# Kernel tuning notes

Measured on AMD Instinct MI355X. Metric: run time of the kernel, lower is better.

## Reference

```python
import jax, jax.numpy as jnp
import numpy as np

B, S, DIM = 2, 2048, 2048
H = 16
Q_LORA, KV_LORA = 768, 512
NOPE, ROPE, VD = 128, 64, 128
QKD = NOPE + ROPE  # 192
SOFTCAP = 30.0
EPS = 1e-6
NEG = -1e9
SCALE = QKD ** -0.5  # max_seq_len <= original_seq_len -> no mscale correction


def rms_norm(x, w, eps=EPS):
    xf = x.astype(jnp.float32)
    y = xf * jax.lax.rsqrt(jnp.mean(xf * xf, axis=-1, keepdims=True) + eps)
    return (y * w.astype(jnp.float32)).astype(x.dtype)


def apply_rope(x, cos, sin):
    # x: [B, S, H, D] with interleaved (even, odd) pairs; cos/sin: [S, D//2]
    xr = x.astype(jnp.float32).reshape(*x.shape[:-1], -1, 2)
    xe, xo = xr[..., 0], xr[..., 1]
    c = cos[None, :, None, :]
    s = sin[None, :, None, :]
    ye = xe * c - xo * s
    yo = xe * s + xo * c
    return jnp.stack([ye, yo], axis=-1).reshape(x.shape).astype(x.dtype)


def setup_inputs():
    key = jax.random.key(0)
    ks = jax.random.split(key, 6)
    def w(k, shape, fan_in):
        return jax.random.normal(k, shape, jnp.float32) * (fan_in ** -0.5)
    x = jax.random.normal(ks[0], (B, S, DIM), jnp.float32)
    wq_a_w = w(ks[1], (Q_LORA, DIM), DIM)
    wq_b_w = w(ks[2], (H * QKD, Q_LORA), Q_LORA)
    wkv_a_w = w(ks[3], (KV_LORA + ROPE, DIM), DIM)
    wkv_b_w = w(ks[4], (H * (NOPE + VD), KV_LORA), KV_LORA)
    wo_w = w(ks[5], (DIM, H * VD), H * VD)
    q_norm_w = jnp.ones((Q_LORA,), jnp.float32)
    kv_norm_w = jnp.ones((KV_LORA,), jnp.float32)
    q_gain = jnp.full((H,), 1.5, jnp.float32)  # qk_gain_init
    inv_freq = 1.0 / (10000.0 ** (np.arange(0, ROPE, 2, dtype=np.float32) / ROPE))
    fr = np.outer(np.arange(S, dtype=np.float32), inv_freq)  # [S, 32]
    freqs_cos = jnp.asarray(np.cos(fr))
    freqs_sin = jnp.asarray(np.sin(fr))
    mask = jnp.asarray(np.where(np.triu(np.ones((S, S), dtype=bool), 1), NEG, 0.0).astype(np.float32))
    return dict(x=x, wq_a_w=wq_a_w, q_norm_w=q_norm_w, wq_b_w=wq_b_w, q_gain=q_gain,
                wkv_a_w=wkv_a_w, kv_norm_w=kv_norm_w, wkv_b_w=wkv_b_w, wo_w=wo_w,
                freqs_cos=freqs_cos, freqs_sin=freqs_sin, mask=mask, start_pos=0)


def reference(x, wq_a_w, q_norm_w, wq_b_w, q_gain, wkv_a_w, kv_norm_w, wkv_b_w, wo_w,
              freqs_cos, freqs_sin, mask, start_pos):
    b, s, _ = x.shape
    # low-rank Q: wq_a -> RMSNorm -> wq_b
    q = rms_norm(x @ wq_a_w.T, q_norm_w) @ wq_b_w.T          # [B,S,H*QKD]
    q = q.reshape(b, s, H, QKD)
    q_nope, q_pe = q[..., :NOPE], q[..., NOPE:]
    q_pe = apply_rope(q_pe, freqs_cos, freqs_sin)            # rope_dims=0 -> full 64-dim rotation
    q_pe = q_pe * q_gain[None, None, :, None]                # learned per-head QK gain
    # low-rank KV + decoupled rope key
    kv_full = x @ wkv_a_w.T                                  # [B,S,KV_LORA+ROPE]
    kv, k_pe = kv_full[..., :KV_LORA], kv_full[..., KV_LORA:]
    kv = rms_norm(kv, kv_norm_w)
    k_pe = apply_rope(k_pe[:, :, None, :], freqs_cos, freqs_sin)  # [B,S,1,ROPE]
    # prefill (mask is not None) branch: expand latent kv through wkv_b
    kvb = (kv @ wkv_b_w.T).reshape(b, s, H, NOPE + VD)
    k_nope, v = kvb[..., :NOPE], kvb[..., NOPE:]
    k = jnp.concatenate([k_nope, jnp.broadcast_to(k_pe, (b, s, H, ROPE))], axis=-1)
    qf = jnp.concatenate([q_nope, q_pe], axis=-1)            # [B,S,H,QKD]
    scores = jnp.einsum('bshd,bthd->bsht', qf, k) * SCALE
    scores = SOFTCAP * jnp.tanh(scores / SOFTCAP)            # logit softcap
    scores = scores + mask[None, :, None, :]                 # causal additive mask [S,T]
    p = jax.nn.softmax(scores.astype(jnp.float32), axis=-1).astype(x.dtype)
    y = jnp.einsum('bsht,bthd->bshd', p, v)                  # [B,S,H,VD]
    # XSA: subtract self-value projection
    vn = v * jax.lax.rsqrt(jnp.maximum(jnp.sum(v * v, axis=-1, keepdims=True), 1e-12))
    y = y - jnp.sum(y * vn, axis=-1, keepdims=True) * vn
    return y.reshape(b, s, H * VD) @ wo_w.T                  # [B,S,DIM]
```

## Files before the change

### kernel.cpp

```cpp
#include <hip/hip_runtime.h>
#include <stdint.h>

typedef unsigned short u16;
typedef __bf16 bf16x8 __attribute__((ext_vector_type(8)));
typedef float f32x4 __attribute__((ext_vector_type(4)));
typedef unsigned int u32x4 __attribute__((ext_vector_type(4)));
typedef unsigned int u32x2 __attribute__((ext_vector_type(2)));

typedef __attribute__((address_space(3))) void LDSV;
typedef __attribute__((address_space(1))) void GLV;

#define S_LEN 2048

__device__ __forceinline__ float bf2f(u16 u) {
  union { unsigned int i; float f; } v; v.i = ((unsigned int)u) << 16; return v.f;
}
__device__ __forceinline__ u16 f2bf(float f) {
  union { float f; unsigned int i; } v; v.f = f;
  unsigned int x = v.i;
  return (u16)((x + 0x7fffu + ((x >> 16) & 1u)) >> 16);
}
__device__ __forceinline__ unsigned int cvtpk(float lo, float hi) {
  unsigned int r;
  asm("v_cvt_pk_bf16_f32 %0, %1, %2" : "=v"(r) : "v"(lo), "v"(hi));
  return r;
}
__device__ __forceinline__ unsigned long long pack4(float4 v) {
  return (unsigned long long)f2bf(v.x)
       | ((unsigned long long)f2bf(v.y) << 16)
       | ((unsigned long long)f2bf(v.z) << 32)
       | ((unsigned long long)f2bf(v.w) << 48);
}

__global__ __launch_bounds__(256) void cast_all(
    const float* __restrict__ s0, u16* __restrict__ d0, long e0,
    const float* __restrict__ s1, u16* __restrict__ d1, long e1,
    const float* __restrict__ s2, u16* __restrict__ d2, long e2,
    const float* __restrict__ s3, u16* __restrict__ d3, long e3,
    const float* __restrict__ s4, u16* __restrict__ d4, long e4,
    const float* __restrict__ s5, u16* __restrict__ d5, long e5) {
  long i = (long)blockIdx.x * 256 + threadIdx.x;
  const float* src; u16* dst; long base; bool pad = false;
  if (i < e0)      { src = s0; dst = d0; base = 0; }
  else if (i < e1) { src = s1; dst = d1; base = e0; }
  else if (i < e2) { src = s2; dst = d2; base = e1; }
  else if (i < e3) { src = s3; dst = d3; base = e2; }
  else if (i < e4) { src = s4; dst = d4; base = e3; }
  else if (i < e5) { src = s5; dst = d5; base = e4; pad = true; }
  else return;
  long li = i - base;
  long elem0 = li * 4;
  unsigned long long r = 0;
  if (!pad || (elem0 >> 11) < 576)
    r = pack4(*(const float4*)(src + elem0));
  ((unsigned long long*)dst)[li] = r;
}

#define MM_PHASE(QM, QN, BB)                                                     \
  __builtin_amdgcn_s_setprio(1);                                                 \
  {                                                                              \
    _Pragma("unroll") for (int mf = 0; mf < 4; ++mf) {                           \
      _Pragma("unroll") for (int nf = 0; nf < 2; ++nf) {                         \
        _Pragma("unroll") for (int kk = 0; kk < 2; ++kk) {                       \
          acc[(QM) * 4 + mf][(QN) * 2 + nf] =                                    \
              __builtin_amdgcn_mfma_f32_16x16x32_bf16(                           \
                  a[mf][kk], BB[nf][kk], acc[(QM) * 4 + mf][(QN) * 2 + nf],      \
                  0, 0, 0);                                                      \
        }                                                                        \
      }                                                                          \
    }                                                                            \
  }                                                                              \
  __builtin_amdgcn_s_setprio(0);

template <int MODE>
__global__ __launch_bounds__(512, 2) void gemm256(const u16* __restrict__ A, int lda,
                                                  const u16* __restrict__ B, int ldb,
                                                  void* __restrict__ Cv, int ldc,
                                                  u16* __restrict__ Vc, int K) {
  __shared__ u16 SMEM[65536];
  const int tid = threadIdx.x;
  const int lane = tid & 63, wid = tid >> 6;
  const int l15 = lane & 15, l4 = lane >> 4;
  const int wm16 = (wid >> 2) * 16, wn16 = (wid & 3) * 16;

  const int gx = gridDim.x, nwg = gx * gridDim.y;
  int lin0 = blockIdx.y * gx + blockIdx.x;
  int cpx = nwg >> 3;
  int swzb = (lin0 & 7) * cpx + (lin0 >> 3);
  const long bm = (long)(swzb / gx) * 256;
  const long bn = (long)(swzb % gx) * 256;

  long aoff[2], boff[2];
#pragma unroll
  for (int j = 0; j < 2; ++j) {
    int lb = (j * 512 + tid) * 16;
    int swz = lb ^ (((lb >> 7) & 7) << 4);
    int sr = swz >> 7, sc = (swz & 127) >> 1;
    aoff[j] = (bm + sr) * (long)lda + sc;
    boff[j] = (bn + sr) * (long)ldb + sc;
  }

  auto STAGE = [&](int buf, int half, int isB, int tt) {
#pragma unroll
    for (int j = 0; j < 2; ++j) {
      const u16* src = isB ? (B + boff[j] + (long)half * 128 * ldb + tt * 64)
                           : (A + aoff[j] + (long)half * 128 * lda + tt * 64);
      __builtin_amdgcn_global_load_lds(
          (const GLV*)src,
          (LDSV*)((char*)SMEM + isB * 65536 + buf * 32768 + half * 16384 +
                  (j * 512 + tid) * 16),
          16, 0, 0);
    }
  };

  f32x4 acc[8][4] = {};
  bf16x8 a[4][2], b0[2][2], b1[2][2];

  auto LDA_ = [&](int buf, int qm) {
#pragma unroll
    for (int mf = 0; mf < 4; ++mf)
#pragma unroll
      for (int kk = 0; kk < 2; ++kk) {
        int r = mf * 32 + wm16 + l15;
        int lb = r * 128 + kk * 64 + l4 * 16;
        a[mf][kk] = *(const bf16x8*)((char*)SMEM + buf * 32768 + qm * 16384 +
                                     (lb ^ ((r & 7) << 4)));
      }
  };
  auto LDB_ = [&](int buf, int qn, bf16x8 (*bb)[2]) {
#pragma unroll
    for (int nf = 0; nf < 2; ++nf)
#pragma unroll
      for (int kk = 0; kk < 2; ++kk) {
        int r = nf * 64 + wn16 + l15;
        int lb = r * 128 + kk * 64 + l4 * 16;
        bb[nf][kk] = *(const bf16x8*)((char*)SMEM + 65536 + buf * 32768 +
                                      qn * 16384 + (lb ^ ((r & 7) << 4)));
      }
  };

  const int NT = K >> 6;
  STAGE(0, 0, 0, 0); STAGE(0, 0, 1, 0); STAGE(0, 1, 1, 0); STAGE(0, 1, 0, 0);
  STAGE(1, 0, 0, 1); STAGE(1, 0, 1, 1);
  asm volatile("s_waitcnt vmcnt(4)" ::: "memory");
  __builtin_amdgcn_s_barrier();

  for (int t = 0; t < NT; ++t) {
    const int cb = t & 1;
    if (t + 1 < NT) STAGE(cb ^ 1, 1, 1, t + 1);
    LDA_(cb, 0);
    LDB_(cb, 0, b0);
    __builtin_amdgcn_s_barrier();
    asm volatile("s_waitcnt lgkmcnt(0)" ::: "memory");
    __builtin_amdgcn_sched_barrier(0);
    MM_PHASE(0, 0, b0);
    __builtin_amdgcn_s_barrier();
    if (t + 1 < NT) STAGE(cb ^ 1, 1, 0, t + 1);
    LDB_(cb, 1, b1);
    __builtin_amdgcn_s_barrier();
    asm volatile("s_waitcnt lgkmcnt(0)" ::: "memory");
    __builtin_amdgcn_sched_barrier(0);
    MM_PHASE(0, 1, b1);
    __builtin_amdgcn_s_barrier();
    if (t + 2 < NT) STAGE(cb, 0, 0, t + 2);
    LDA_(cb, 1);
    __builtin_amdgcn_s_barrier();
    asm volatile("s_waitcnt lgkmcnt(0)" ::: "memory");
    __builtin_amdgcn_sched_barrier(0);
    MM_PHASE(1, 0, b0);
    __builtin_amdgcn_s_barrier();
    if (t + 2 < NT) STAGE(cb, 0, 1, t + 2);
    __builtin_amdgcn_s_barrier();
    MM_PHASE(1, 1, b1);
    if (t + 2 < NT) asm volatile("s_waitcnt vmcnt(4)" ::: "memory");
    else            asm volatile("s_waitcnt vmcnt(0)" ::: "memory");
    __builtin_amdgcn_s_barrier();
  }

#pragma unroll
  for (int mfg = 0; mfg < 8; ++mfg)
#pragma unroll
    for (int nfg = 0; nfg < 4; ++nfg)
#pragma unroll
      for (int r = 0; r < 4; ++r) {
        long row = bm + mfg * 32 + wm16 + l4 * 4 + r;
        long col = bn + nfg * 64 + wn16 + l15;
        float v = acc[mfg][nfg][r];
        if constexpr (MODE == 0) {
          ((u16*)Cv)[row * ldc + col] = f2bf(v);
        } else if constexpr (MODE == 1) {
          ((float*)Cv)[row * ldc + col] = v;
        } else {
          int h = (int)(col >> 8), c = (int)(col & 255);
          if (c < 128)
            ((u16*)Cv)[(((row >> 11) * 16 + h) * 2048 + (row & 2047)) * 128 + c] = f2bf(v);
          else
            Vc[row * 2048 + h * 128 + (c - 128)] = f2bf(v);
        }
      }
}

#define MM_TALL(QM, QN, BB)                                                      \
  __builtin_amdgcn_s_setprio(1);                                                 \
  {                                                                              \
    _Pragma("unroll") for (int mf = 0; mf < 4; ++mf) {                           \
      _Pragma("unroll") for (int kk = 0; kk < 2; ++kk) {                         \
        acc[(QM) * 4 + mf][(QN)] = __builtin_amdgcn_mfma_f32_16x16x32_bf16(      \
            a[mf][kk], BB[kk], acc[(QM) * 4 + mf][(QN)], 0, 0, 0);               \
      }                                                                          \
    }                                                                            \
  }                                                                              \
  __builtin_amdgcn_s_setprio(0);

template <int MODE>
__global__ __launch_bounds__(512, 2) void gemm_tall(const u16* __restrict__ A, int lda,
                                                    const u16* __restrict__ B, int ldb,
                                                    void* __restrict__ Cv, int ldc,
                                                    u16* __restrict__ Vc, int K) {
  __shared__ u16 SMEM[49152];
  const int tid = threadIdx.x;
  const int lane = tid & 63, wid = tid >> 6;
  const int l15 = lane & 15, l4 = lane >> 4;
  const int wm16 = (wid >> 2) * 16, wn16 = (wid & 3) * 16;

  const int gx = gridDim.x, nwg = gx * gridDim.y;
  int lin0 = blockIdx.y * gx + blockIdx.x;
  int cpx = nwg >> 3;
  int swzb = (lin0 & 7) * cpx + (lin0 >> 3);
  const long bm = (long)(swzb / gx) * 256;
  const long bn = (long)(swzb % gx) * 128;

  long aoff[2], boffv;
#pragma unroll
  for (int j = 0; j < 2; ++j) {
    int lb = (j * 512 + tid) * 16;
    int swz = lb ^ (((lb >> 7) & 7) << 4);
    aoff[j] = (bm + (swz >> 7)) * (long)lda + ((swz & 127) >> 1);
  }
  {
    int lb = tid * 16;
    int swz = lb ^ (((lb >> 7) & 7) << 4);
    boffv = (bn + (swz >> 7)) * (long)ldb + ((swz & 127) >> 1);
  }

  auto SA = [&](int buf, int half, int tt) {
#pragma unroll
    for (int j = 0; j < 2; ++j)
      __builtin_amdgcn_global_load_lds(
          (const GLV*)(A + aoff[j] + (long)half * 128 * lda + tt * 64),
          (LDSV*)((char*)SMEM + buf * 32768 + half * 16384 + (j * 512 + tid) * 16),
          16, 0, 0);
  };
  auto SB = [&](int buf, int half, int tt) {
    __builtin_amdgcn_global_load_lds(
        (const GLV*)(B + boffv + (long)half * 64 * ldb + tt * 64),
        (LDSV*)((char*)SMEM + 65536 + buf * 16384 + half * 8192 + tid * 16),
        16, 0, 0);
  };

  f32x4 acc[8][2] = {};
  bf16x8 a[4][2], b0[2], b1[2];

  auto LDA_ = [&](int buf, int qm) {
#pragma unroll
    for (int mf = 0; mf < 4; ++mf)
#pragma unroll
      for (int kk = 0; kk < 2; ++kk) {
        int r = mf * 32 + wm16 + l15;
        int lb = r * 128 + kk * 64 + l4 * 16;
        a[mf][kk] = *(const bf16x8*)((char*)SMEM + buf * 32768 + qm * 16384 +
                                     (lb ^ ((r & 7) << 4)));
      }
  };
  auto LDB_ = [&](int buf, int qn, bf16x8* bb) {
#pragma unroll
    for (int kk = 0; kk < 2; ++kk) {
      int r = wn16 + l15;
      int lb = r * 128 + kk * 64 + l4 * 16;
      bb[kk] = *(const bf16x8*)((char*)SMEM + 65536 + buf * 16384 + qn * 8192 +
                                (lb ^ ((r & 7) << 4)));
    }
  };

  const int NT = K >> 6;
  SA(0, 0, 0); SB(0, 0, 0); SB(0, 1, 0); SA(0, 1, 0);
  SA(1, 0, 1); SB(1, 0, 1);
  asm volatile("s_waitcnt vmcnt(3)" ::: "memory");
  __builtin_amdgcn_s_barrier();

  for (int t = 0; t < NT; ++t) {
    const int cb = t & 1;
    if (t + 1 < NT) SB(cb ^ 1, 1, t + 1);
    LDA_(cb, 0);
    LDB_(cb, 0, b0);
    __builtin_amdgcn_s_barrier();
    asm volatile("s_waitcnt lgkmcnt(0)" ::: "memory");
    __builtin_amdgcn_sched_barrier(0);
    MM_TALL(0, 0, b0);
    __builtin_amdgcn_s_barrier();
    if (t + 1 < NT) SA(cb ^ 1, 1, t + 1);
    LDB_(cb, 1, b1);
    __builtin_amdgcn_s_barrier();
    asm volatile("s_waitcnt lgkmcnt(0)" ::: "memory");
    __builtin_amdgcn_sched_barrier(0);
    MM_TALL(0, 1, b1);
    __builtin_amdgcn_s_barrier();
    if (t + 2 < NT) SA(cb, 0, t + 2);
    LDA_(cb, 1);
    __builtin_amdgcn_s_barrier();
    asm volatile("s_waitcnt lgkmcnt(0)" ::: "memory");
    __builtin_amdgcn_sched_barrier(0);
    MM_TALL(1, 0, b0);
    __builtin_amdgcn_s_barrier();
    if (t + 2 < NT) SB(cb, 0, t + 2);
    __builtin_amdgcn_s_barrier();
    MM_TALL(1, 1, b1);
    if (t + 2 < NT) asm volatile("s_waitcnt vmcnt(6)" ::: "memory");
    else            asm volatile("s_waitcnt vmcnt(0)" ::: "memory");
    __builtin_amdgcn_s_barrier();
  }

#pragma unroll
  for (int mfg = 0; mfg < 8; ++mfg)
#pragma unroll
    for (int qn = 0; qn < 2; ++qn)
#pragma unroll
      for (int r = 0; r < 4; ++r) {
        long row = bm + mfg * 32 + wm16 + l4 * 4 + r;
        long col = bn + qn * 64 + wn16 + l15;
        float v = acc[mfg][qn][r];
        if constexpr (MODE == 0) {
          ((u16*)Cv)[row * ldc + col] = f2bf(v);
        } else if constexpr (MODE == 1) {
          ((float*)Cv)[row * ldc + col] = v;
        } else {
          int h = (int)(col >> 8), c = (int)(col & 255);
          if (c < 128)
            ((u16*)Cv)[(((row >> 11) * 16 + h) * 2048 + (row & 2047)) * 128 + c] = f2bf(v);
          else
            Vc[row * 2048 + h * 128 + (c - 128)] = f2bf(v);
        }
      }
}

__global__ __launch_bounds__(256) void rmsnorm2_kernel(u16* __restrict__ qakv,
                                                       const float* __restrict__ qw,
                                                       const float* __restrict__ kvw) {
  __shared__ float sred[4];
  const int tid = threadIdx.x;
  const int row = blockIdx.x;
  if (row < 4096) {
    u16* p = qakv + (size_t)row * 1408;
    float x[3];
    float ss = 0.f;
#pragma unroll
    for (int i = 0; i < 3; ++i) { x[i] = bf2f(p[tid + i * 256]); ss += x[i] * x[i]; }
#pragma unroll
    for (int off = 1; off < 64; off <<= 1) ss += __shfl_xor(ss, off);
    if ((tid & 63) == 0) sred[tid >> 6] = ss;
    __syncthreads();
    float tot = sred[0] + sred[1] + sred[2] + sred[3];
    float rs = rsqrtf(tot * (1.0f / 768.0f) + 1e-6f) * 0.0069411711f;
#pragma unroll
    for (int i = 0; i < 3; ++i) p[tid + i * 256] = f2bf(x[i] * rs * qw[tid + i * 256]);
  } else {
    u16* p = qakv + (size_t)(row - 4096) * 1408 + 768;
    float x[2];
    float ss = 0.f;
#pragma unroll
    for (int i = 0; i < 2; ++i) { x[i] = bf2f(p[tid + i * 256]); ss += x[i] * x[i]; }
#pragma unroll
    for (int off = 1; off < 64; off <<= 1) ss += __shfl_xor(ss, off);
    if ((tid & 63) == 0) sred[tid >> 6] = ss;
    __syncthreads();
    float tot = sred[0] + sred[1] + sred[2] + sred[3];
    float rs = rsqrtf(tot * (1.0f / 512.0f) + 1e-6f);
#pragma unroll
    for (int i = 0; i < 2; ++i) p[tid + i * 256] = f2bf(x[i] * rs * kvw[tid + i * 256]);
  }
}

__global__ __launch_bounds__(256) void ropek_kernel(const u16* __restrict__ qakv,
                                                    const float* __restrict__ cosb,
                                                    const float* __restrict__ sinb,
                                                    u16* __restrict__ kpe) {
  int idx = blockIdx.x * 256 + threadIdx.x;
  int i = idx & 31;
  int srow = idx >> 5;
  int s = srow & 2047;
  unsigned int v = *(const unsigned int*)(qakv + (size_t)srow * 1408 + 1280 + 2 * i);
  float xe = bf2f((u16)(v & 0xffff)), xo = bf2f((u16)(v >> 16));
  float c = cosb[s * 32 + i], sn = sinb[s * 32 + i];
  *(unsigned int*)(kpe + (size_t)srow * 64 + 2 * i) =
      (unsigned int)f2bf(xe * c - xo * sn) | ((unsigned int)f2bf(xe * sn + xo * c) << 16);
}

__global__ __launch_bounds__(256) void v_transpose_kernel(const u16* __restrict__ Vc,
                                                          u16* __restrict__ VT) {
  __shared__ u16 tile[64][65];
  int bh = blockIdx.z;
  int d0 = blockIdx.y * 64;
  int t0 = blockIdx.x * 64;
  int b = bh >> 4, h = bh & 15;
#pragma unroll
  for (int i = 0; i < 2; ++i) {
    int flat = i * 256 + threadIdx.x;
    int t = flat >> 3, c = (flat & 7) * 8;
    u32x4 v = *(const u32x4*)(Vc + ((long)b * S_LEN + t0 + t) * 2048 + h * 128 + d0 + c);
    const u16* pv = (const u16*)&v;
#pragma unroll
    for (int j = 0; j < 8; ++j) tile[c + j][t] = pv[j];
  }
  __syncthreads();
#pragma unroll
  for (int i = 0; i < 2; ++i) {
    int flat = i * 256 + threadIdx.x;
    int d = flat >> 3, tc = (flat & 7) * 8;
    u32x4 v;
    u16* pv = (u16*)&v;
#pragma unroll
    for (int j = 0; j < 8; ++j) pv[j] = tile[d][tc + j];
    *(u32x4*)(VT + ((long)bh * 128 + d0 + d) * S_LEN + t0 + tc) = v;
  }
}

__global__ __launch_bounds__(512, 2) void attn_kernel(const u16* __restrict__ Qg,
                                                      const u16* __restrict__ KbN,
                                                      const u16* __restrict__ Kpe,
                                                      const u16* __restrict__ VTg,
                                                      const u16* __restrict__ Vcg,
                                                      const float* __restrict__ cosb,
                                                      const float* __restrict__ sinb,
                                                      const float* __restrict__ gain,
                                                      u16* __restrict__ Yg) {
  __shared__ u16 Ks[2][64 * 192];
  __shared__ u16 VTs[2][128 * 64];
  __shared__ u16 Ps[128 * 64];

  const int tid = threadIdx.x, lane = tid & 63, wid = tid >> 6;
  const int l15 = lane & 15, l4 = lane >> 4;

  const int p = blockIdx.x;
  const int bh = (p & 7) * 4 + (p >> 6);
  const int pair = (p >> 3) & 7;
  const int b = bh >> 4, h = bh & 15;

  const u16* Kn = KbN + (long)bh * S_LEN * 128;
  const u16* Kp = Kpe + (long)b * S_LEN * 64;
  const u16* Vbh = VTg + (long)bh * 128 * S_LEN;

  int krow[3], sst[3], ksoff[3];
  const u16* sb[3];
#pragma unroll
  for (int i = 0; i < 3; ++i) {
    int flat = i * 512 + tid;
    int r = flat / 24, c = flat % 24;
    krow[i] = r;
    if (c < 16) { sb[i] = Kn + c * 8; sst[i] = 128; }
    else        { sb[i] = Kp + (c - 16) * 8; sst[i] = 64; }
    ksoff[i] = r * 192 + ((c ^ (r & 7)) * 8);
  }
  int vrow[2], vc[2], vsoff[2];
#pragma unroll
  for (int i = 0; i < 2; ++i) {
    int flat = i * 512 + tid;
    vrow[i] = flat >> 3; vc[i] = flat & 7;
    vsoff[i] = vrow[i] * 64 + ((vc[i] ^ (vrow[i] & 7)) * 8);
  }

  const int prow = wid * 16 + l15;
  const int pr7 = prow & 7;
  const float g = gain[h];

  for (int seg = 0; seg < 2; ++seg) {
    const int qt = seg ? pair : 15 - pair;
    const int q0 = qt * 128;
    const int nkt = 2 * qt + 2;
    const int sq = q0 + prow;

    bf16x8 qf[6];
    {
      const u16* qb_ = Qg + ((long)b * S_LEN + sq) * 3072 + h * 192;
#pragma unroll
      for (int f = 0; f < 6; ++f) qf[f] = *(const bf16x8*)(qb_ + f * 32 + 8 * l4);
    }
#pragma unroll
    for (int f = 4; f < 6; ++f) {
      float4 cv = *(const float4*)(cosb + sq * 32 + (f - 4) * 16 + l4 * 4);
      float4 sv = *(const float4*)(sinb + sq * 32 + (f - 4) * 16 + l4 * 4);
      float cc[4] = {cv.x, cv.y, cv.z, cv.w};
      float ssn[4] = {sv.x, sv.y, sv.z, sv.w};
      u16* pq = (u16*)&qf[f];
#pragma unroll
      for (int pp = 0; pp < 4; ++pp) {
        float xe = bf2f(pq[2 * pp]), xo = bf2f(pq[2 * pp + 1]);
        pq[2 * pp]     = f2bf((xe * cc[pp] - xo * ssn[pp]) * g);
        pq[2 * pp + 1] = f2bf((xe * ssn[pp] + xo * cc[pp]) * g);
      }
    }

    f32x4 o[8] = {};
    float lsum = 0.f;

    u32x4 ka[3], va[2];
#pragma unroll
    for (int i = 0; i < 3; ++i)
      ka[i] = *(const u32x4*)(sb[i] + (long)krow[i] * sst[i]);
#pragma unroll
    for (int i = 0; i < 2; ++i)
      va[i] = *(const u32x4*)(Vbh + (long)vrow[i] * S_LEN + vc[i] * 8);
#pragma unroll
    for (int i = 0; i < 3; ++i) *(u32x4*)(&Ks[0][ksoff[i]]) = ka[i];
#pragma unroll
    for (int i = 0; i < 2; ++i) *(u32x4*)(&VTs[0][vsoff[i]]) = va[i];
    if (nkt > 1) {
#pragma unroll
      for (int i = 0; i < 3; ++i)
        ka[i] = *(const u32x4*)(sb[i] + (long)(64 + krow[i]) * sst[i]);
#pragma unroll
      for (int i = 0; i < 2; ++i)
        va[i] = *(const u32x4*)(Vbh + (long)vrow[i] * S_LEN + 64 + vc[i] * 8);
    }
    __syncthreads();

    for (int it = 0; it < nkt; ++it) {
      const int cur = it & 1;

      f32x4 sacc[4] = {};
      __builtin_amdgcn_s_setprio(1);
#pragma unroll
      for (int f = 0; f < 6; ++f)
#pragma unroll
        for (int tf = 0; tf < 4; ++tf) {
          int row = tf * 16 + l15;
          bf16x8 kf = *(const bf16x8*)(&Ks[cur][row * 192 + (((f * 4 + l4) ^ (row & 7)) * 8)]);
          sacc[tf] = __builtin_amdgcn_mfma_f32_16x16x32_bf16(kf, qf[f], sacc[tf], 0, 0, 0);
        }
      __builtin_amdgcn_s_setprio(0);

      if (it + 1 < nkt) {
#pragma unroll
        for (int i = 0; i < 3; ++i) *(u32x4*)(&Ks[cur ^ 1][ksoff[i]]) = ka[i];
#pragma unroll
        for (int i = 0; i < 2; ++i) *(u32x4*)(&VTs[cur ^ 1][vsoff[i]]) = va[i];
      }
      if (it + 2 < nkt) {
        int k0n = (it + 2) * 64;
#pragma unroll
        for (int i = 0; i < 3; ++i)
          ka[i] = *(const u32x4*)(sb[i] + (long)(k0n + krow[i]) * sst[i]);
#pragma unroll
        for (int i = 0; i < 2; ++i)
          va[i] = *(const u32x4*)(Vbh + (long)vrow[i] * S_LEN + k0n + vc[i] * 8);
      }

#pragma unroll
      for (int tf = 0; tf < 4; ++tf)
#pragma unroll
        for (int r = 0; r < 4; ++r) {
          float u = __builtin_amdgcn_exp2f(sacc[tf][r]);
          sacc[tf][r] = __builtin_amdgcn_exp2f(-86.56170245333781f *
                                               __builtin_amdgcn_rcpf(u + 1.0f));
        }
      if (it * 64 >= q0) {
        const int dthr = q0 + prow - it * 64 - l4 * 4;
#pragma unroll
        for (int tf = 0; tf < 4; ++tf)
#pragma unroll
          for (int r = 0; r < 4; ++r)
            if (tf * 16 + r > dthr) sacc[tf][r] = 0.f;
      }
#pragma unroll
      for (int tf = 0; tf < 4; ++tf)
#pragma unroll
        for (int r = 0; r < 4; ++r) lsum += sacc[tf][r];

#pragma unroll
      for (int tf = 0; tf < 4; ++tf) {
        u32x2 w;
        w.x = cvtpk(sacc[tf][0], sacc[tf][1]);
        w.y = cvtpk(sacc[tf][2], sacc[tf][3]);
        int chunk = tf * 2 + (l4 >> 1);
        *(u32x2*)(&Ps[prow * 64 + ((chunk ^ pr7) * 8) + (l4 & 1) * 4]) = w;
      }

      __builtin_amdgcn_s_setprio(1);
#pragma unroll
      for (int kk = 0; kk < 2; ++kk) {
        bf16x8 pf = *(const bf16x8*)(&Ps[prow * 64 + (((kk * 4 + l4) ^ pr7) * 8)]);
#pragma unroll
        for (int nf = 0; nf < 8; ++nf) {
          int vr = nf * 16 + l15;
          bf16x8 vf = *(const bf16x8*)(&VTs[cur][vr * 64 + (((kk * 4 + l4) ^ (vr & 7)) * 8)]);
          o[nf] = __builtin_amdgcn_mfma_f32_16x16x32_bf16(pf, vf, o[nf], 0, 0, 0);
        }
      }
      __builtin_amdgcn_s_setprio(0);

      __syncthreads();
    }

    lsum += __shfl_xor(lsum, 16);
    lsum += __shfl_xor(lsum, 32);
    float inv[4];
#pragma unroll
    for (int r = 0; r < 4; ++r)
      inv[r] = __builtin_amdgcn_rcpf(__shfl(lsum, l4 * 4 + r));

    float yv[8][4], vvv[8][4];
    float ssum[4] = {0.f, 0.f, 0.f, 0.f}, dsum[4] = {0.f, 0.f, 0.f, 0.f};
    const u16* vb = Vcg + ((long)b * S_LEN + q0 + wid * 16) * 2048 + h * 128;
#pragma unroll
    for (int nf = 0; nf < 8; ++nf)
#pragma unroll
      for (int r = 0; r < 4; ++r) {
        float vv = bf2f(vb[(l4 * 4 + r) * 2048 + nf * 16 + l15]);
        float y = o[nf][r] * inv[r];
        vvv[nf][r] = vv; yv[nf][r] = y;
        ssum[r] += vv * vv; dsum[r] += y * vv;
      }
#pragma unroll
    for (int r = 0; r < 4; ++r) {
      ssum[r] += __shfl_xor(ssum[r], 1); ssum[r] += __shfl_xor(ssum[r], 2);
      ssum[r] += __shfl_xor(ssum[r], 4); ssum[r] += __shfl_xor(ssum[r], 8);
      dsum[r] += __shfl_xor(dsum[r], 1); dsum[r] += __shfl_xor(dsum[r], 2);
      dsum[r] += __shfl_xor(dsum[r], 4); dsum[r] += __shfl_xor(dsum[r], 8);
      dsum[r] *= __builtin_amdgcn_rcpf(fmaxf(ssum[r], 1e-12f));
    }
#pragma unroll
    for (int nf = 0; nf < 8; ++nf)
#pragma unroll
      for (int r = 0; r < 4; ++r) {
        long row = (long)b * S_LEN + q0 + wid * 16 + l4 * 4 + r;
        Yg[row * 2048 + h * 128 + nf * 16 + l15] = f2bf(yv[nf][r] - dsum[r] * vvv[nf][r]);
      }
  }
}

extern "C" void kernel_launch(void* const* d_in, const int* in_sizes, int n_in,
                              void* d_out, int out_size, void* d_ws, size_t ws_size,
                              hipStream_t stream) {
  const float* x       = (const float*)d_in[0];
  const float* wq_a    = (const float*)d_in[1];
  const float* q_norm  = (const float*)d_in[2];
  const float* wq_b    = (const float*)d_in[3];
  const float* q_gain  = (const float*)d_in[4];
  const float* wkv_a   = (const float*)d_in[5];
  const float* kv_norm = (const float*)d_in[6];
  const float* wkv_b   = (const float*)d_in[7];
  const float* wo      = (const float*)d_in[8];
  const float* fcos    = (const float*)d_in[9];
  const float* fsin    = (const float*)d_in[10];
  float* out = (float*)d_out;

  char* ws = (char*)d_ws;
  size_t off = 0;
  auto alloc = [&](size_t bytes) {
    char* pp = ws + off;
    off += (bytes + 255) & ~(size_t)255;
    return pp;
  };
  const long M = 4096;
  u16* xb    = (u16*)alloc(M * 2048 * 2);
  u16* wcomb = (u16*)alloc(1408L * 2048 * 2);
  u16* wqbb  = (u16*)alloc(3072L * 768 * 2);
  u16* wkvbb = (u16*)alloc(4096L * 512 * 2);
  u16* wob   = (u16*)alloc(2048L * 2048 * 2);
  u16* qakv  = (u16*)alloc(M * 1408 * 2);
  u16* qb    = (u16*)alloc(M * 3072 * 2);
  u16* KbN   = (u16*)alloc(32L * 2048 * 128 * 2);
  u16* kpe   = (u16*)alloc(M * 64 * 2);
  u16* Vc    = (u16*)alloc(M * 2048 * 2);
  u16* VTb   = (u16*)alloc(32L * 128 * 2048 * 2);
  u16* Yb    = (u16*)alloc(M * 2048 * 2);

  const long n4_x = 2097152, n4_wqa = 393216, n4_wqb = 589824,
             n4_wkvb = 524288, n4_wo = 1048576, n4_wkvap = 327680;
  long e0 = n4_x, e1 = e0 + n4_wqa, e2 = e1 + n4_wqb, e3 = e2 + n4_wkvb,
       e4 = e3 + n4_wo, e5 = e4 + n4_wkvap;
  cast_all<<<(int)(e5 / 256), 256, 0, stream>>>(
      x, xb, e0, wq_a, wcomb, e1, wq_b, wqbb, e2, wkv_b, wkvbb, e3,
      wo, wob, e4, wkv_a, wcomb + 768L * 2048, e5);

  gemm_tall<0><<<dim3(11, 16), 512, 0, stream>>>(xb, 2048, wcomb, 2048, qakv, 1408, nullptr, 2048);
  rmsnorm2_kernel<<<8192, 256, 0, stream>>>(qakv, q_norm, kv_norm);
  gemm256<0><<<dim3(12, 16), 512, 0, stream>>>(qakv, 1408, wqbb, 768, qb, 3072, nullptr, 768);
  ropek_kernel<<<131072 / 256, 256, 0, stream>>>(qakv, fcos, fsin, kpe);
  gemm256<2><<<dim3(16, 16), 512, 0, stream>>>(qakv + 768, 1408, wkvbb, 512, KbN, 0, Vc, 512);
  v_transpose_kernel<<<dim3(32, 2, 32), 256, 0, stream>>>(Vc, VTb);
  attn_kernel<<<256, 512, 0, stream>>>(qb, KbN, kpe, VTb, Vc, fcos, fsin, q_gain, Yb);
  gemm_tall<1><<<dim3(16, 16), 512, 0, stream>>>(Yb, 2048, wob, 2048, out, 2048, nullptr, 2048);
}
```

Baseline: 238.4 us.

## Split attention warps into two KV-tile groups with 32-row query tiles and combine

Each warp now owns 32 query rows (two MFMA row fragments) so every K and V fragment read from LDS feeds two MFMAs. The 8 warps are split into two groups that process alternating 64-key tiles, and their partial outputs and row sums are merged through shared memory at the end. This halves the iteration count and LDS reads per MFMA, at the cost of dropping double-buffered LDS staging (two barriers per iteration), more registers, and occupancy lowered to one block per CU.

```diff
diff --git a/kernel.cpp b/kernel.cpp
--- a/kernel.cpp
+++ b/kernel.cpp
@@ -424,7 +424,7 @@
   }
 }
 
-__global__ __launch_bounds__(512, 2) void attn_kernel(const u16* __restrict__ Qg,
+__global__ __launch_bounds__(512, 1) void attn_kernel(const u16* __restrict__ Qg,
                                                       const u16* __restrict__ KbN,
                                                       const u16* __restrict__ Kpe,
                                                       const u16* __restrict__ VTg,
@@ -433,12 +433,14 @@
                                                       const float* __restrict__ sinb,
                                                       const float* __restrict__ gain,
                                                       u16* __restrict__ Yg) {
-  __shared__ u16 Ks[2][64 * 192];
-  __shared__ u16 VTs[2][128 * 64];
-  __shared__ u16 Ps[128 * 64];
+  __shared__ u16 SM[57344];
+  u16* Kbase = SM;
+  u16* Vbase = SM + 24576;
+  u16* Pbase = SM + 40960;
 
   const int tid = threadIdx.x, lane = tid & 63, wid = tid >> 6;
   const int l15 = lane & 15, l4 = lane >> 4;
+  const int grp = wid >> 2, gw = wid & 3;
 
   const int p = blockIdx.x;
   const int bh = (p & 7) * 4 + (p >> 6);
@@ -449,191 +451,228 @@
   const u16* Kp = Kpe + (long)b * S_LEN * 64;
   const u16* Vbh = VTg + (long)bh * 128 * S_LEN;
 
-  int krow[3], sst[3], ksoff[3];
-  const u16* sb[3];
-#pragma unroll
-  for (int i = 0; i < 3; ++i) {
+  int kt_[6], krow_[6], kstr[6], ksoff[6];
+  const u16* ksb[6];
+#pragma unroll
+  for (int i = 0; i < 6; ++i) {
     int flat = i * 512 + tid;
-    int r = flat / 24, c = flat % 24;
-    krow[i] = r;
-    if (c < 16) { sb[i] = Kn + c * 8; sst[i] = 128; }
-    else        { sb[i] = Kp + (c - 16) * 8; sst[i] = 64; }
-    ksoff[i] = r * 192 + ((c ^ (r & 7)) * 8);
-  }
-  int vrow[2], vc[2], vsoff[2];
-#pragma unroll
-  for (int i = 0; i < 2; ++i) {
+    int kt = flat / 1536, idx = flat % 1536;
+    int r = idx / 24, c = idx % 24;
+    kt_[i] = kt; krow_[i] = r;
+    if (c < 16) { ksb[i] = Kn + c * 8; kstr[i] = 128; }
+    else        { ksb[i] = Kp + (c - 16) * 8; kstr[i] = 64; }
+    ksoff[i] = kt * 12288 + r * 192 + ((c ^ (r & 7)) * 8);
+  }
+  int vt_[4], vrow_[4], vc_[4], vsoff[4];
+#pragma unroll
+  for (int i = 0; i < 4; ++i) {
     int flat = i * 512 + tid;
-    vrow[i] = flat >> 3; vc[i] = flat & 7;
-    vsoff[i] = vrow[i] * 64 + ((vc[i] ^ (vrow[i] & 7)) * 8);
-  }
-
-  const int prow = wid * 16 + l15;
-  const int pr7 = prow & 7;
+    int vt = flat >> 10, idx = flat & 1023;
+    int vr = idx >> 3, vcc = idx & 7;
+    vt_[i] = vt; vrow_[i] = vr; vc_[i] = vcc;
+    vsoff[i] = 24576 + vt * 8192 + vr * 64 + ((vcc ^ (vr & 7)) * 8);
+  }
+
+  u16* Kbuf = Kbase + grp * 12288;
+  u16* Vbuf = Vbase + grp * 8192;
+  u16* Pbuf = Pbase + grp * 8192;
+  const int rowp0 = gw * 32 + l15;
   const float g = gain[h];
 
   for (int seg = 0; seg < 2; ++seg) {
     const int qt = seg ? pair : 15 - pair;
     const int q0 = qt * 128;
-    const int nkt = 2 * qt + 2;
-    const int sq = q0 + prow;
-
-    bf16x8 qf[6];
-    {
+    const int niter = qt + 1;
+
+    bf16x8 qf[2][6];
+#pragma unroll
+    for (int mf = 0; mf < 2; ++mf) {
+      const int sq = q0 + rowp0 + mf * 16;
       const u16* qb_ = Qg + ((long)b * S_LEN + sq) * 3072 + h * 192;
 #pragma unroll
-      for (int f = 0; f < 6; ++f) qf[f] = *(const bf16x8*)(qb_ + f * 32 + 8 * l4);
+      for (int f = 0; f < 6; ++f) qf[mf][f] = *(const bf16x8*)(qb_ + f * 32 + 8 * l4);
+#pragma unroll
+      for (int f = 4; f < 6; ++f) {
+        float4 cv = *(const float4*)(cosb + sq * 32 + (f - 4) * 16 + l4 * 4);
+        float4 sv = *(const float4*)(sinb + sq * 32 + (f - 4) * 16 + l4 * 4);
+        float cc[4] = {cv.x, cv.y, cv.z, cv.w};
+        float ssn[4] = {sv.x, sv.y, sv.z, sv.w};
+        u16* pq = (u16*)&qf[mf][f];
+#pragma unroll
+        for (int pp = 0; pp < 4; ++pp) {
+          float xe = bf2f(pq[2 * pp]), xo = bf2f(pq[2 * pp + 1]);
+          pq[2 * pp]     = f2bf((xe * cc[pp] - xo * ssn[pp]) * g);
+          pq[2 * pp + 1] = f2bf((xe * ssn[pp] + xo * cc[pp]) * g);
+        }
+      }
     }
-#pragma unroll
-    for (int f = 4; f < 6; ++f) {
-      float4 cv = *(const float4*)(cosb + sq * 32 + (f - 4) * 16 + l4 * 4);
-      float4 sv = *(const float4*)(sinb + sq * 32 + (f - 4) * 16 + l4 * 4);
-      float cc[4] = {cv.x, cv.y, cv.z, cv.w};
-      float ssn[4] = {sv.x, sv.y, sv.z, sv.w};
-      u16* pq = (u16*)&qf[f];
-#pragma unroll
-      for (int pp = 0; pp < 4; ++pp) {
-        float xe = bf2f(pq[2 * pp]), xo = bf2f(pq[2 * pp + 1]);
-        pq[2 * pp]     = f2bf((xe * cc[pp] - xo * ssn[pp]) * g);
-        pq[2 * pp + 1] = f2bf((xe * ssn[pp] + xo * cc[pp]) * g);
-      }
+
+    f32x4 o[2][8] = {};
+    float lsum[2] = {0.f, 0.f};
+
+    u32x4 ka[6], va[4];
+#pragma unroll
+    for (int i = 0; i < 6; ++i)
+      ka[i] = *(const u32x4*)(ksb[i] + (long)(kt_[i] * 64 + krow_[i]) * kstr[i]);
+#pragma unroll
+    for (int i = 0; i < 4; ++i)
+      va[i] = *(const u32x4*)(Vbh + (long)vrow_[i] * S_LEN + vt_[i] * 64 + vc_[i] * 8);
+
+    for (int it = 0; it < niter; ++it) {
+      __syncthreads();
+#pragma unroll
+      for (int i = 0; i < 6; ++i) *(u32x4*)(&SM[ksoff[i]]) = ka[i];
+#pragma unroll
+      for (int i = 0; i < 4; ++i) *(u32x4*)(&SM[vsoff[i]]) = va[i];
+      __syncthreads();
+      if (it + 1 < niter) {
+        const int t2 = 2 * (it + 1);
+#pragma unroll
+        for (int i = 0; i < 6; ++i)
+          ka[i] = *(const u32x4*)(ksb[i] + (long)((t2 + kt_[i]) * 64 + krow_[i]) * kstr[i]);
+#pragma unroll
+        for (int i = 0; i < 4; ++i)
+          va[i] = *(const u32x4*)(Vbh + (long)vrow_[i] * S_LEN + (t2 + vt_[i]) * 64 + vc_[i] * 8);
+      }
+
+      const int tt = 2 * it + grp;
+
+      f32x4 sacc[2][4] = {};
+      __builtin_amdgcn_s_setprio(1);
+#pragma unroll
+      for (int f = 0; f < 6; ++f)
+#pragma unroll
+        for (int tf = 0; tf < 4; ++tf) {
+          int row = tf * 16 + l15;
+          bf16x8 kf = *(const bf16x8*)(&Kbuf[row * 192 + (((f * 4 + l4) ^ (row & 7)) * 8)]);
+          sacc[0][tf] = __builtin_amdgcn_mfma_f32_16x16x32_bf16(kf, qf[0][f], sacc[0][tf], 0, 0, 0);
+          sacc[1][tf] = __builtin_amdgcn_mfma_f32_16x16x32_bf16(kf, qf[1][f], sacc[1][tf], 0, 0, 0);
+        }
+      __builtin_amdgcn_s_setprio(0);
+
+#pragma unroll
+      for (int mf = 0; mf < 2; ++mf)
+#pragma unroll
+        for (int tf = 0; tf < 4; ++tf)
+#pragma unroll
+          for (int r = 0; r < 4; ++r) {
+            float u = __builtin_amdgcn_exp2f(sacc[mf][tf][r]);
+            sacc[mf][tf][r] = __builtin_amdgcn_exp2f(-86.56170245333781f *
+                                                     __builtin_amdgcn_rcpf(u + 1.0f));
+          }
+      if (tt * 64 >= q0) {
+#pragma unroll
+        for (int mf = 0; mf < 2; ++mf) {
+          const int dthr = q0 + rowp0 + mf * 16 - tt * 64 - l4 * 4;
+#pragma unroll
+          for (int tf = 0; tf < 4; ++tf)
+#pragma unroll
+            for (int r = 0; r < 4; ++r)
+              if (tf * 16 + r > dthr) sacc[mf][tf][r] = 0.f;
+        }
+      }
+#pragma unroll
+      for (int mf = 0; mf < 2; ++mf)
+#pragma unroll
+        for (int tf = 0; tf < 4; ++tf)
+#pragma unroll
+          for (int r = 0; r < 4; ++r) lsum[mf] += sacc[mf][tf][r];
+
+#pragma unroll
+      for (int mf = 0; mf < 2; ++mf) {
+        const int rp = rowp0 + mf * 16, rp7 = rp & 7;
+#pragma unroll
+        for (int tf = 0; tf < 4; ++tf) {
+          u32x2 w;
+          w.x = cvtpk(sacc[mf][tf][0], sacc[mf][tf][1]);
+          w.y = cvtpk(sacc[mf][tf][2], sacc[mf][tf][3]);
+          int chunk = tf * 2 + (l4 >> 1);
+          *(u32x2*)(&Pbuf[rp * 64 + ((chunk ^ rp7) * 8) + (l4 & 1) * 4]) = w;
+        }
+      }
+
+      __builtin_amdgcn_s_setprio(1);
+#pragma unroll
+      for (int kk = 0; kk < 2; ++kk) {
+        bf16x8 pf[2];
+#pragma unroll
+        for (int mf = 0; mf < 2; ++mf) {
+          const int rp = rowp0 + mf * 16, rp7 = rp & 7;
+          pf[mf] = *(const bf16x8*)(&Pbuf[rp * 64 + (((kk * 4 + l4) ^ rp7) * 8)]);
+        }
+#pragma unroll
+        for (int nf = 0; nf < 8; ++nf) {
+          int vr = nf * 16 + l15;
+          bf16x8 vf = *(const bf16x8*)(&Vbuf[vr * 64 + (((kk * 4 + l4) ^ (vr & 7)) * 8)]);
+          o[0][nf] = __builtin_amdgcn_mfma_f32_16x16x32_bf16(pf[0], vf, o[0][nf], 0, 0, 0);
+          o[1][nf] = __builtin_amdgcn_mfma_f32_16x16x32_bf16(pf[1], vf, o[1][nf], 0, 0, 0);
+        }
+      }
+      __builtin_amdgcn_s_setprio(0);
     }
 
-    f32x4 o[8] = {};
-    float lsum = 0.f;
-
-    u32x4 ka[3], va[2];
-#pragma unroll
-    for (int i = 0; i < 3; ++i)
-      ka[i] = *(const u32x4*)(sb[i] + (long)krow[i] * sst[i]);
-#pragma unroll
-    for (int i = 0; i < 2; ++i)
-      va[i] = *(const u32x4*)(Vbh + (long)vrow[i] * S_LEN + vc[i] * 8);
-#pragma unroll
-    for (int i = 0; i < 3; ++i) *(u32x4*)(&Ks[0][ksoff[i]]) = ka[i];
-#pragma unroll
-    for (int i = 0; i < 2; ++i) *(u32x4*)(&VTs[0][vsoff[i]]) = va[i];
-    if (nkt > 1) {
-#pragma unroll
-      for (int i = 0; i < 3; ++i)
-        ka[i] = *(const u32x4*)(sb[i] + (long)(64 + krow[i]) * sst[i]);
-#pragma unroll
-      for (int i = 0; i < 2; ++i)
-        va[i] = *(const u32x4*)(Vbh + (long)vrow[i] * S_LEN + 64 + vc[i] * 8);
+#pragma unroll
+    for (int mf = 0; mf < 2; ++mf) {
+      lsum[mf] += __shfl_xor(lsum[mf], 16);
+      lsum[mf] += __shfl_xor(lsum[mf], 32);
+    }
+
+    __syncthreads();
+    float* OL = (float*)SM;
+    float* LL = (float*)(SM + 40960);
+    if (grp == 1) {
+#pragma unroll
+      for (int mf = 0; mf < 2; ++mf) {
+#pragma unroll
+        for (int nf = 0; nf < 8; ++nf)
+#pragma unroll
+          for (int r = 0; r < 4; ++r)
+            OL[(gw * 32 + mf * 16 + l4 * 4 + r) * 128 + nf * 16 + l15] = o[mf][nf][r];
+        if (l4 == 0) LL[gw * 32 + mf * 16 + l15] = lsum[mf];
+      }
     }
     __syncthreads();
-
-    for (int it = 0; it < nkt; ++it) {
-      const int cur = it & 1;
-
-      f32x4 sacc[4] = {};
-      __builtin_amdgcn_s_setprio(1);
-#pragma unroll
-      for (int f = 0; f < 6; ++f)
-#pragma unroll
-        for (int tf = 0; tf < 4; ++tf) {
-          int row = tf * 16 + l15;
-          bf16x8 kf = *(const bf16x8*)(&Ks[cur][row * 192 + (((f * 4 + l4) ^ (row & 7)) * 8)]);
-          sacc[tf] = __builtin_amdgcn_mfma_f32_16x16x32_bf16(kf, qf[f], sacc[tf], 0, 0, 0);
-        }
-      __builtin_amdgcn_s_setprio(0);
-
-      if (it + 1 < nkt) {
-#pragma unroll
-        for (int i = 0; i < 3; ++i) *(u32x4*)(&Ks[cur ^ 1][ksoff[i]]) = ka[i];
-#pragma unroll
-        for (int i = 0; i < 2; ++i) *(u32x4*)(&VTs[cur ^ 1][vsoff[i]]) = va[i];
-      }
-      if (it + 2 < nkt) {
-        int k0n = (it + 2) * 64;
-#pragma unroll
-        for (int i = 0; i < 3; ++i)
-          ka[i] = *(const u32x4*)(sb[i] + (long)(k0n + krow[i]) * sst[i]);
-#pragma unroll
-        for (int i = 0; i < 2; ++i)
-          va[i] = *(const u32x4*)(Vbh + (long)vrow[i] * S_LEN + k0n + vc[i] * 8);
-      }
-
-#pragma unroll
-      for (int tf = 0; tf < 4; ++tf)
+    if (grp == 0) {
+#pragma unroll
+      for (int mf = 0; mf < 2; ++mf) {
+        lsum[mf] += LL[gw * 32 + mf * 16 + l15];
+        float inv[4];
+#pragma unroll
+        for (int r = 0; r < 4; ++r)
+          inv[r] = __builtin_amdgcn_rcpf(__shfl(lsum[mf], l4 * 4 + r));
+
+        float yv[8][4], vvv[8][4];
+        float ssum[4] = {0.f, 0.f, 0.f, 0.f}, dsum[4] = {0.f, 0.f, 0.f, 0.f};
+        const u16* vb = Vcg + ((long)b * S_LEN + q0 + gw * 32 + mf * 16) * 2048 + h * 128;
+#pragma unroll
+        for (int nf = 0; nf < 8; ++nf)
+#pragma unroll
+          for (int r = 0; r < 4; ++r) {
+            float ov = o[mf][nf][r] +
+                       OL[(gw * 32 + mf * 16 + l4 * 4 + r) * 128 + nf * 16 + l15];
+            float vv = bf2f(vb[(l4 * 4 + r) * 2048 + nf * 16 + l15]);
+            float y = ov * inv[r];
+            vvv[nf][r] = vv; yv[nf][r] = y;
+            ssum[r] += vv * vv; dsum[r] += y * vv;
+          }
 #pragma unroll
         for (int r = 0; r < 4; ++r) {
-          float u = __builtin_amdgcn_exp2f(sacc[tf][r]);
-          sacc[tf][r] = __builtin_amdgcn_exp2f(-86.56170245333781f *
-                                               __builtin_amdgcn_rcpf(u + 1.0f));
-        }
-      if (it * 64 >= q0) {
-        const int dthr = q0 + prow - it * 64 - l4 * 4;
-#pragma unroll
-        for (int tf = 0; tf < 4; ++tf)
-#pragma unroll
-          for (int r = 0; r < 4; ++r)
-            if (tf * 16 + r > dthr) sacc[tf][r] = 0.f;
-      }
-#pragma unroll
-      for (int tf = 0; tf < 4; ++tf)
-#pragma unroll
-        for (int r = 0; r < 4; ++r) lsum += sacc[tf][r];
-
-#pragma unroll
-      for (int tf = 0; tf < 4; ++tf) {
-        u32x2 w;
-        w.x = cvtpk(sacc[tf][0], sacc[tf][1]);
-        w.y = cvtpk(sacc[tf][2], sacc[tf][3]);
-        int chunk = tf * 2 + (l4 >> 1);
-        *(u32x2*)(&Ps[prow * 64 + ((chunk ^ pr7) * 8) + (l4 & 1) * 4]) = w;
-      }
-
-      __builtin_amdgcn_s_setprio(1);
-#pragma unroll
-      for (int kk = 0; kk < 2; ++kk) {
-        bf16x8 pf = *(const bf16x8*)(&Ps[prow * 64 + (((kk * 4 + l4) ^ pr7) * 8)]);
-#pragma unroll
-        for (int nf = 0; nf < 8; ++nf) {
-          int vr = nf * 16 + l15;
-          bf16x8 vf = *(const bf16x8*)(&VTs[cur][vr * 64 + (((kk * 4 + l4) ^ (vr & 7)) * 8)]);
-          o[nf] = __builtin_amdgcn_mfma_f32_16x16x32_bf16(pf, vf, o[nf], 0, 0, 0);
-        }
-      }
-      __builtin_amdgcn_s_setprio(0);
-
-      __syncthreads();
+          ssum[r] += __shfl_xor(ssum[r], 1); ssum[r] += __shfl_xor(ssum[r], 2);
+          ssum[r] += __shfl_xor(ssum[r], 4); ssum[r] += __shfl_xor(ssum[r], 8);
+          dsum[r] += __shfl_xor(dsum[r], 1); dsum[r] += __shfl_xor(dsum[r], 2);
+          dsum[r] += __shfl_xor(dsum[r], 4); dsum[r] += __shfl_xor(dsum[r], 8);
+          dsum[r] *= __builtin_amdgcn_rcpf(fmaxf(ssum[r], 1e-12f));
+        }
+#pragma unroll
+        for (int nf = 0; nf < 8; ++nf)
+#pragma unroll
+          for (int r = 0; r < 4; ++r) {
+            long row = (long)b * S_LEN + q0 + gw * 32 + mf * 16 + l4 * 4 + r;
+            Yg[row * 2048 + h * 128 + nf * 16 + l15] =
+                f2bf(yv[nf][r] - dsum[r] * vvv[nf][r]);
+          }
+      }
     }
-
-    lsum += __shfl_xor(lsum, 16);
-    lsum += __shfl_xor(lsum, 32);
-    float inv[4];
-#pragma unroll
-    for (int r = 0; r < 4; ++r)
-      inv[r] = __builtin_amdgcn_rcpf(__shfl(lsum, l4 * 4 + r));
-
-    float yv[8][4], vvv[8][4];
-    float ssum[4] = {0.f, 0.f, 0.f, 0.f}, dsum[4] = {0.f, 0.f, 0.f, 0.f};
-    const u16* vb = Vcg + ((long)b * S_LEN + q0 + wid * 16) * 2048 + h * 128;
-#pragma unroll
-    for (int nf = 0; nf < 8; ++nf)
-#pragma unroll
-      for (int r = 0; r < 4; ++r) {
-        float vv = bf2f(vb[(l4 * 4 + r) * 2048 + nf * 16 + l15]);
-        float y = o[nf][r] * inv[r];
-        vvv[nf][r] = vv; yv[nf][r] = y;
-        ssum[r] += vv * vv; dsum[r] += y * vv;
-      }
-#pragma unroll
-    for (int r = 0; r < 4; ++r) {
-      ssum[r] += __shfl_xor(ssum[r], 1); ssum[r] += __shfl_xor(ssum[r], 2);
-      ssum[r] += __shfl_xor(ssum[r], 4); ssum[r] += __shfl_xor(ssum[r], 8);
-      dsum[r] += __shfl_xor(dsum[r], 1); dsum[r] += __shfl_xor(dsum[r], 2);
-      dsum[r] += __shfl_xor(dsum[r], 4); dsum[r] += __shfl_xor(dsum[r], 8);
-      dsum[r] *= __builtin_amdgcn_rcpf(fmaxf(ssum[r], 1e-12f));
-    }
-#pragma unroll
-    for (int nf = 0; nf < 8; ++nf)
-#pragma unroll
-      for (int r = 0; r < 4; ++r) {
-        long row = (long)b * S_LEN + q0 + wid * 16 + l4 * 4 + r;
-        Yg[row * 2048 + h * 128 + nf * 16 + l15] = f2bf(yv[nf][r] - dsum[r] * vvv[nf][r]);
-      }
   }
 }
 
```

After: 297.7 us. +24.8%, slower.

## Stage attention K/V tiles with direct global-to-LDS loads; fuse K rope into rmsnorm

Applied to the files above, without the earlier changes.

The attention kernel now copies K and V^T tiles straight from global memory into LDS with global_load_lds, replacing the register-staged prefetch. To keep the XOR swizzle, the swizzle moves from the LDS destination to the global source address. The next tile's load is issued at the top of each iteration so it overlaps the QK MFMAs, and the held staging registers are freed. Separately, the k_pe rope kernel is folded into the kv branch of rmsnorm2, removing one launch; the risk is whether the async LDS writes are properly waited on before the buffer is reused.

```diff
diff --git a/kernel.cpp b/kernel.cpp
--- a/kernel.cpp
+++ b/kernel.cpp
@@ -345,7 +345,10 @@
 
 __global__ __launch_bounds__(256) void rmsnorm2_kernel(u16* __restrict__ qakv,
                                                        const float* __restrict__ qw,
-                                                       const float* __restrict__ kvw) {
+                                                       const float* __restrict__ kvw,
+                                                       const float* __restrict__ cosb,
+                                                       const float* __restrict__ sinb,
+                                                       u16* __restrict__ kpe) {
   __shared__ float sred[4];
   const int tid = threadIdx.x;
   const int row = blockIdx.x;
@@ -364,7 +367,8 @@
 #pragma unroll
     for (int i = 0; i < 3; ++i) p[tid + i * 256] = f2bf(x[i] * rs * qw[tid + i * 256]);
   } else {
-    u16* p = qakv + (size_t)(row - 4096) * 1408 + 768;
+    const int srow = row - 4096;
+    u16* p = qakv + (size_t)srow * 1408 + 768;
     float x[2];
     float ss = 0.f;
 #pragma unroll
@@ -377,22 +381,15 @@
     float rs = rsqrtf(tot * (1.0f / 512.0f) + 1e-6f);
 #pragma unroll
     for (int i = 0; i < 2; ++i) p[tid + i * 256] = f2bf(x[i] * rs * kvw[tid + i * 256]);
-  }
-}
-
-__global__ __launch_bounds__(256) void ropek_kernel(const u16* __restrict__ qakv,
-                                                    const float* __restrict__ cosb,
-                                                    const float* __restrict__ sinb,
-                                                    u16* __restrict__ kpe) {
-  int idx = blockIdx.x * 256 + threadIdx.x;
-  int i = idx & 31;
-  int srow = idx >> 5;
-  int s = srow & 2047;
-  unsigned int v = *(const unsigned int*)(qakv + (size_t)srow * 1408 + 1280 + 2 * i);
-  float xe = bf2f((u16)(v & 0xffff)), xo = bf2f((u16)(v >> 16));
-  float c = cosb[s * 32 + i], sn = sinb[s * 32 + i];
-  *(unsigned int*)(kpe + (size_t)srow * 64 + 2 * i) =
-      (unsigned int)f2bf(xe * c - xo * sn) | ((unsigned int)f2bf(xe * sn + xo * c) << 16);
+    if (tid < 32) {
+      int s = srow & 2047;
+      unsigned int v = *(const unsigned int*)(qakv + (size_t)srow * 1408 + 1280 + 2 * tid);
+      float xe = bf2f((u16)(v & 0xffff)), xo = bf2f((u16)(v >> 16));
+      float c = cosb[s * 32 + tid], sn = sinb[s * 32 + tid];
+      *(unsigned int*)(kpe + (size_t)srow * 64 + 2 * tid) =
+          (unsigned int)f2bf(xe * c - xo * sn) | ((unsigned int)f2bf(xe * sn + xo * c) << 16);
+    }
+  }
 }
 
 __global__ __launch_bounds__(256) void v_transpose_kernel(const u16* __restrict__ Vc,
@@ -449,23 +446,25 @@
   const u16* Kp = Kpe + (long)b * S_LEN * 64;
   const u16* Vbh = VTg + (long)bh * 128 * S_LEN;
 
-  int krow[3], sst[3], ksoff[3];
-  const u16* sb[3];
+  int krow[3], kstr[3], kdst[3];
+  const u16* ksrc[3];
 #pragma unroll
   for (int i = 0; i < 3; ++i) {
-    int flat = i * 512 + tid;
-    int r = flat / 24, c = flat % 24;
+    int flat = (i * 512 + tid) * 8;
+    int r = flat / 192, cs = (flat % 192) >> 3;
+    int c = cs ^ (r & 7);
     krow[i] = r;
-    if (c < 16) { sb[i] = Kn + c * 8; sst[i] = 128; }
-    else        { sb[i] = Kp + (c - 16) * 8; sst[i] = 64; }
-    ksoff[i] = r * 192 + ((c ^ (r & 7)) * 8);
-  }
-  int vrow[2], vc[2], vsoff[2];
+    if (c < 16) { ksrc[i] = Kn + c * 8; kstr[i] = 128; }
+    else        { ksrc[i] = Kp + (c - 16) * 8; kstr[i] = 64; }
+    kdst[i] = flat;
+  }
+  int vrow[2], vcc[2], vdst[2];
 #pragma unroll
   for (int i = 0; i < 2; ++i) {
-    int flat = i * 512 + tid;
-    vrow[i] = flat >> 3; vc[i] = flat & 7;
-    vsoff[i] = vrow[i] * 64 + ((vc[i] ^ (vrow[i] & 7)) * 8);
+    int flat = (i * 512 + tid) * 8;
+    int r = flat / 64, cs = (flat % 64) >> 3;
+    vrow[i] = r; vcc[i] = cs ^ (r & 7);
+    vdst[i] = flat;
   }
 
   const int prow = wid * 16 + l15;
@@ -477,6 +476,19 @@
     const int q0 = qt * 128;
     const int nkt = 2 * qt + 2;
     const int sq = q0 + prow;
+
+    auto STAGEKV = [&](int buf, int k0) {
+#pragma unroll
+      for (int i = 0; i < 3; ++i)
+        __builtin_amdgcn_global_load_lds(
+            (const GLV*)(ksrc[i] + (long)(k0 + krow[i]) * kstr[i]),
+            (LDSV*)(&Ks[buf][kdst[i]]), 16, 0, 0);
+#pragma unroll
+      for (int i = 0; i < 2; ++i)
+        __builtin_amdgcn_global_load_lds(
+            (const GLV*)(Vbh + (long)vrow[i] * S_LEN + k0 + vcc[i] * 8),
+            (LDSV*)(&VTs[buf][vdst[i]]), 16, 0, 0);
+    };
 
     bf16x8 qf[6];
     {
@@ -502,29 +514,12 @@
     f32x4 o[8] = {};
     float lsum = 0.f;
 
-    u32x4 ka[3], va[2];
-#pragma unroll
-    for (int i = 0; i < 3; ++i)
-      ka[i] = *(const u32x4*)(sb[i] + (long)krow[i] * sst[i]);
-#pragma unroll
-    for (int i = 0; i < 2; ++i)
-      va[i] = *(const u32x4*)(Vbh + (long)vrow[i] * S_LEN + vc[i] * 8);
-#pragma unroll
-    for (int i = 0; i < 3; ++i) *(u32x4*)(&Ks[0][ksoff[i]]) = ka[i];
-#pragma unroll
-    for (int i = 0; i < 2; ++i) *(u32x4*)(&VTs[0][vsoff[i]]) = va[i];
-    if (nkt > 1) {
-#pragma unroll
-      for (int i = 0; i < 3; ++i)
-        ka[i] = *(const u32x4*)(sb[i] + (long)(64 + krow[i]) * sst[i]);
-#pragma unroll
-      for (int i = 0; i < 2; ++i)
-        va[i] = *(const u32x4*)(Vbh + (long)vrow[i] * S_LEN + 64 + vc[i] * 8);
-    }
+    STAGEKV(0, 0);
     __syncthreads();
 
     for (int it = 0; it < nkt; ++it) {
       const int cur = it & 1;
+      if (it + 1 < nkt) STAGEKV(cur ^ 1, (it + 1) * 64);
 
       f32x4 sacc[4] = {};
       __builtin_amdgcn_s_setprio(1);
@@ -537,22 +532,6 @@
           sacc[tf] = __builtin_amdgcn_mfma_f32_16x16x32_bf16(kf, qf[f], sacc[tf], 0, 0, 0);
         }
       __builtin_amdgcn_s_setprio(0);
-
-      if (it + 1 < nkt) {
-#pragma unroll
-        for (int i = 0; i < 3; ++i) *(u32x4*)(&Ks[cur ^ 1][ksoff[i]]) = ka[i];
-#pragma unroll
-        for (int i = 0; i < 2; ++i) *(u32x4*)(&VTs[cur ^ 1][vsoff[i]]) = va[i];
-      }
-      if (it + 2 < nkt) {
-        int k0n = (it + 2) * 64;
-#pragma unroll
-        for (int i = 0; i < 3; ++i)
-          ka[i] = *(const u32x4*)(sb[i] + (long)(k0n + krow[i]) * sst[i]);
-#pragma unroll
-        for (int i = 0; i < 2; ++i)
-          va[i] = *(const u32x4*)(Vbh + (long)vrow[i] * S_LEN + k0n + vc[i] * 8);
-      }
 
 #pragma unroll
       for (int tf = 0; tf < 4; ++tf)
@@ -683,9 +662,8 @@
       wo, wob, e4, wkv_a, wcomb + 768L * 2048, e5);
 
   gemm_tall<0><<<dim3(11, 16), 512, 0, stream>>>(xb, 2048, wcomb, 2048, qakv, 1408, nullptr, 2048);
-  rmsnorm2_kernel<<<8192, 256, 0, stream>>>(qakv, q_norm, kv_norm);
+  rmsnorm2_kernel<<<8192, 256, 0, stream>>>(qakv, q_norm, kv_norm, fcos, fsin, kpe);
   gemm256<0><<<dim3(12, 16), 512, 0, stream>>>(qakv, 1408, wqbb, 768, qb, 3072, nullptr, 768);
-  ropek_kernel<<<131072 / 256, 256, 0, stream>>>(qakv, fcos, fsin, kpe);
   gemm256<2><<<dim3(16, 16), 512, 0, stream>>>(qakv + 768, 1408, wkvbb, 512, KbN, 0, Vc, 512);
   v_transpose_kernel<<<dim3(32, 2, 32), 256, 0, stream>>>(Vc, VTb);
   attn_kernel<<<256, 512, 0, stream>>>(qb, KbN, kpe, VTb, Vc, fcos, fsin, q_gain, Yb);
```

New measurement: 246.8 us. 3.5% more time.
